# Performance work log

Hardware: AMD Instinct MI355X
Metric: run time of the kernel (lower is better)

Reference implementation:

```python
import jax, jax.numpy as jnp
import numpy as np

D_MODEL = 1024
EXPAND = 2
D_INNER = EXPAND * D_MODEL          # 2048
D_STATE = 64
NGROUPS = 1
HEADDIM = 128
NHEADS = D_INNER // HEADDIM         # 16
D_CONV = 4
CONV_DIM = D_INNER + 2 * NGROUPS * D_STATE      # 2176
D_IN_PROJ = 2 * D_INNER + 2 * NGROUPS * D_STATE + NHEADS  # 4240
BATCH = 2
SEQLEN = 4096
RMS_EPS = 1e-5


def setup_inputs() -> dict:
    key = jax.random.key(0)
    ks = jax.random.split(key, 8)
    u = jax.random.normal(ks[0], (BATCH, SEQLEN, D_MODEL), jnp.float32)
    in_proj_w = jax.random.normal(ks[1], (D_IN_PROJ, D_MODEL), jnp.float32) * 0.02
    conv_w = jax.random.normal(ks[2], (CONV_DIM, D_CONV), jnp.float32) * 0.2
    conv_b = jax.random.normal(ks[3], (CONV_DIM,), jnp.float32) * 0.1
    dt_bias = jax.random.normal(ks[4], (NHEADS,), jnp.float32) * 0.5
    # A ~ Uniform(1,16), A_log = log(A)  (as in Mamba2 init)
    A_log = jnp.log(jax.random.uniform(ks[5], (NHEADS,), jnp.float32, 1.0, 16.0))
    D = jnp.ones((NHEADS,), jnp.float32)
    rms_w = jnp.ones((D_INNER,), jnp.float32)
    out_w = jax.random.normal(ks[6], (D_MODEL, D_INNER), jnp.float32) * 0.02
    return {"u": u, "in_proj_w": in_proj_w, "conv_w": conv_w, "conv_b": conv_b,
            "dt_bias": dt_bias, "A_log": A_log, "D": D, "rms_w": rms_w, "out_w": out_w}


def reference(u, in_proj_w, conv_w, conv_b, dt_bias, A_log, D, rms_w, out_w):
    Bsz, L, _ = u.shape
    # in_proj: (B,L,d_model) -> (B,L,d_in_proj), split [z, x, B, C, dt]
    zxbcdt = jnp.einsum('bld,ed->ble', u, in_proj_w)
    s1 = D_INNER
    s2 = 2 * D_INNER
    s3 = s2 + NGROUPS * D_STATE
    s4 = s3 + NGROUPS * D_STATE
    z = zxbcdt[..., :s1]
    x = zxbcdt[..., s1:s2]
    B_part = zxbcdt[..., s2:s3]
    C_part = zxbcdt[..., s3:s4]
    dt = zxbcdt[..., s4:]
    dt = jax.nn.softplus(dt + dt_bias)            # (B,L,H), dt_limit=(0,inf) -> no clamp

    # depthwise causal conv1d + silu over [x, B, C]
    xBC = jnp.concatenate([x, B_part, C_part], axis=-1)      # (B,L,CONV_DIM)
    xt = xBC.transpose(0, 2, 1)                              # (B,C,L)
    kern = conv_w[:, None, :]                                # (C,1,W)
    conv = jax.lax.conv_general_dilated(
        xt, kern, (1,), [(D_CONV - 1, 0)],
        dimension_numbers=('NCH', 'OIH', 'NCH'),
        feature_group_count=CONV_DIM)
    xBC = jax.nn.silu((conv + conv_b[None, :, None]).transpose(0, 2, 1))

    x_c = xBC[..., :D_INNER]
    B_c = xBC[..., D_INNER:D_INNER + NGROUPS * D_STATE]
    C_c = xBC[..., D_INNER + NGROUPS * D_STATE:]
    x_s = x_c.reshape(Bsz, L, NHEADS, HEADDIM)               # (B,L,H,P)
    hpg = NHEADS // NGROUPS
    B_full = jnp.repeat(B_c.reshape(Bsz, L, NGROUPS, D_STATE), hpg, axis=2)  # (B,L,H,N)
    C_full = jnp.repeat(C_c.reshape(Bsz, L, NGROUPS, D_STATE), hpg, axis=2)

    A = -jnp.exp(A_log)                                      # (H,)

    def step(state, inp):
        x_t, dt_t, B_t, C_t = inp  # (B,H,P),(B,H),(B,H,N),(B,H,N)
        decay = jnp.exp(dt_t * A)[:, :, None, None]          # (B,H,1,1)
        state = decay * state + B_t[:, :, None, :] * x_t[..., None]  # (B,H,P,N)
        y_t = jnp.einsum('bhpn,bhn->bhp', state, C_t)
        return state, y_t

    init = jnp.zeros((Bsz, NHEADS, HEADDIM, D_STATE), u.dtype)
    xs = (x_s.transpose(1, 0, 2, 3), dt.transpose(1, 0, 2),
          B_full.transpose(1, 0, 2, 3), C_full.transpose(1, 0, 2, 3))
    _, ys = jax.lax.scan(step, init, xs)                     # (L,B,H,P)
    y = ys.transpose(1, 0, 2, 3) + D[None, None, :, None] * x_s

    y_flat = y.reshape(Bsz, L, D_INNER)
    mu = jnp.mean(y_flat * y_flat, axis=-1, keepdims=True)
    y_flat = y_flat * jax.lax.rsqrt(mu + RMS_EPS) * rms_w    # RMSNorm
    y_flat = y_flat * jax.nn.sigmoid(z)                      # gate
    return jnp.einsum('bld,ed->ble', y_flat, out_w)          # out_proj (no bias)
```

## Files before the change

kernel.cpp:

```cpp
#include <hip/hip_runtime.h>
#include <math.h>

#define D_MODEL   1024
#define D_INNER   2048
#define D_STATE   64
#define HEADDIM   128
#define NHEADS    16
#define D_CONV    4
#define BATCH     2
#define SEQLEN    4096
#define RMS_EPS   1e-5f
#define D_IN_PROJ 4240

#define ZX_LD     4224

#define LCHUNK    128
#define NCHUNK    (SEQLEN / LCHUNK)

typedef __attribute__((ext_vector_type(8))) short short8;
typedef __attribute__((ext_vector_type(4))) float f32x4;
typedef _Float16 half8 __attribute__((ext_vector_type(8)));

__device__ __forceinline__ ushort f2bf(float f) {
  unsigned u = __float_as_uint(f);
  u += 0x7fff + ((u >> 16) & 1);
  return (ushort)(u >> 16);
}
__device__ __forceinline__ float bf2f(ushort h) {
  return __uint_as_float(((unsigned)h) << 16);
}
__device__ __forceinline__ ushort f2h(float f) {
  _Float16 h = (_Float16)f;
  ushort u; __builtin_memcpy(&u, &h, 2); return u;
}
__device__ __forceinline__ void ld4(const float* p, float* d) {
  float4 v = *(const float4*)p; d[0] = v.x; d[1] = v.y; d[2] = v.z; d[3] = v.w;
}
__device__ __forceinline__ void ld4b(const ushort* p, float* d) {
  ushort4 v = *(const ushort4*)p;
  d[0] = bf2f(v.x); d[1] = bf2f(v.y); d[2] = bf2f(v.z); d[3] = bf2f(v.w);
}

__device__ __forceinline__ void gl_lds16(const ushort* g, ushort* l) {
  __builtin_amdgcn_global_load_lds(
      (const __attribute__((address_space(1))) unsigned int*)g,
      (__attribute__((address_space(3))) unsigned int*)l, 16, 0, 0);
}

__global__ void cvt_split(const float* __restrict__ w,
                          ushort* __restrict__ hi, ushort* __restrict__ lo, int n4) {
  int i = blockIdx.x * 256 + threadIdx.x;
  if (i >= n4) return;
  float4 v = ((const float4*)w)[i];
  ushort h0 = f2bf(v.x), h1 = f2bf(v.y), h2 = f2bf(v.z), h3 = f2bf(v.w);
  ushort l0 = f2bf(v.x - bf2f(h0)), l1 = f2bf(v.y - bf2f(h1));
  ushort l2 = f2bf(v.z - bf2f(h2)), l3 = f2bf(v.w - bf2f(h3));
  ((ushort4*)hi)[i] = make_ushort4(h0, h1, h2, h3);
  ((ushort4*)lo)[i] = make_ushort4(l0, l1, l2, l3);
}

__global__ void cvt_f16(const float* __restrict__ w, ushort* __restrict__ o, int n4) {
  int i = blockIdx.x * 256 + threadIdx.x;
  if (i >= n4) return;
  float4 v = ((const float4*)w)[i];
  ((ushort4*)o)[i] = make_ushort4(f2h(v.x), f2h(v.y), f2h(v.z), f2h(v.w));
}

template<int BM, int BK, bool ALO, bool OBF16>
__launch_bounds__(256, 3)
__global__ void gemm_bf16p(const ushort* __restrict__ Ah, const ushort* __restrict__ Al,
                           const ushort* __restrict__ Bh, const ushort* __restrict__ Bl,
                           float* __restrict__ C, int ldc,
                           int M, int N, int ldab, int Kslice, int n1term) {
  constexpr int BN = 128;
  constexpr int NQ = BK / 8;
  constexpr int RT = BM / 32;
  constexpr int CT = 4;
  constexpr int KS = BK / 32;

  __shared__ ushort As[ALO ? 2 : 1][BM * BK];
  __shared__ ushort Bs[2][BN * BK];

  const int bn   = blockIdx.x * BN;
  if (bn >= N) return;
  const bool two = (bn >= n1term);
  const int t    = threadIdx.x;
  const int bm   = blockIdx.y * BM;
  const int kz   = blockIdx.z;
  const int kb   = kz * Kslice;
  C += (size_t)kz * M * ldc;
  const int wave = t >> 6, lane = t & 63;
  const int ml   = lane & 15, g4 = lane >> 4;
  const int sw   = ml & (NQ - 1);
  const int wr   = wave & 1, wc = wave >> 1;
  const int r0   = wr * RT * 16, c0 = wc * CT * 16;

  f32x4 acc[RT][CT];
#pragma unroll
  for (int i = 0; i < RT; ++i)
#pragma unroll
    for (int j = 0; j < CT; ++j) acc[i][j] = (f32x4){0.f, 0.f, 0.f, 0.f};

  for (int k0 = kb; k0 < kb + Kslice; k0 += BK) {
    __syncthreads();
#pragma unroll
    for (int ii = 0; ii < BM * NQ / 256; ++ii) {
      int idx = t + ii * 256;
      int row = idx / NQ, qs = idx % NQ;
      int qg  = qs ^ (row & (NQ - 1));
      size_t go = (size_t)(bm + row) * ldab + k0 + qg * 8;
      gl_lds16(Ah + go, &As[0][idx * 8]);
      if (ALO) gl_lds16(Al + go, &As[ALO ? 1 : 0][idx * 8]);
    }
#pragma unroll
    for (int ii = 0; ii < BN * NQ / 256; ++ii) {
      int idx = t + ii * 256;
      int row = idx / NQ, qs = idx % NQ;
      int qg  = qs ^ (row & (NQ - 1));
      size_t go = (size_t)(bn + row) * ldab + k0 + qg * 8;
      gl_lds16(Bh + go, &Bs[0][idx * 8]);
      if (two) gl_lds16(Bl + go, &Bs[1][idx * 8]);
    }
    __syncthreads();

#pragma unroll
    for (int ks = 0; ks < KS; ++ks) {
      const int qA = ((ks * 4 + g4) ^ sw) * 8;
      short8 ah[RT], al[RT], bh[CT], bl[CT];
#pragma unroll
      for (int i = 0; i < RT; ++i) {
        int off = (r0 + i * 16 + ml) * BK + qA;
        ah[i] = *(const short8*)&As[0][off];
        if (ALO) al[i] = *(const short8*)&As[ALO ? 1 : 0][off];
      }
#pragma unroll
      for (int j = 0; j < CT; ++j) {
        int off = (c0 + j * 16 + ml) * BK + qA;
        bh[j] = *(const short8*)&Bs[0][off];
        if (two) bl[j] = *(const short8*)&Bs[1][off];
      }
#pragma unroll
      for (int i = 0; i < RT; ++i)
#pragma unroll
        for (int j = 0; j < CT; ++j) {
          acc[i][j] = __builtin_amdgcn_mfma_f32_16x16x32_bf16(ah[i], bh[j], acc[i][j], 0, 0, 0);
          if (two)
            acc[i][j] = __builtin_amdgcn_mfma_f32_16x16x32_bf16(ah[i], bl[j], acc[i][j], 0, 0, 0);
          if (ALO)
            acc[i][j] = __builtin_amdgcn_mfma_f32_16x16x32_bf16(al[i], bh[j], acc[i][j], 0, 0, 0);
        }
    }
  }

#pragma unroll
  for (int i = 0; i < RT; ++i)
#pragma unroll
    for (int j = 0; j < CT; ++j) {
      int col = bn + c0 + j * 16 + ml;
      if (col < N) {
        int rowb = bm + r0 + i * 16 + g4 * 4;
#pragma unroll
        for (int r = 0; r < 4; ++r) {
          if (OBF16) ((ushort*)C)[(size_t)(rowb + r) * ldc + col] = f2bf(acc[i][j][r]);
          else       C[(size_t)(rowb + r) * ldc + col] = acc[i][j][r];
        }
      }
    }
}

template<int BM, int BK, bool OBF16, bool PIPE>
__launch_bounds__(256, PIPE ? 2 : 4)
__global__ void gemm_f16(const ushort* __restrict__ Ah, const ushort* __restrict__ Bh,
                         float* __restrict__ C, int ldc,
                         int M, int N, int ldab, int Kslice) {
  constexpr int BN = 128;
  constexpr int NQ = BK / 8;
  constexpr int RT = BM / 32;
  constexpr int CT = 4;
  constexpr int KS = BK / 32;
  constexpr int NBUF = PIPE ? 2 : 1;

  __shared__ ushort As[NBUF][BM * BK];
  __shared__ ushort Bs[NBUF][BN * BK];

  const int bn   = blockIdx.x * BN;
  if (bn >= N) return;
  const int t    = threadIdx.x;
  const int bm   = blockIdx.y * BM;
  const int kz   = blockIdx.z;
  const int kb   = kz * Kslice;
  C += (size_t)kz * M * ldc;
  const int wave = t >> 6, lane = t & 63;
  const int ml   = lane & 15, g4 = lane >> 4;
  const int sw   = ml & (NQ - 1);
  const int wr   = wave & 1, wc = wave >> 1;
  const int r0   = wr * RT * 16, c0 = wc * CT * 16;

  f32x4 acc[RT][CT];
#pragma unroll
  for (int i = 0; i < RT; ++i)
#pragma unroll
    for (int j = 0; j < CT; ++j) acc[i][j] = (f32x4){0.f, 0.f, 0.f, 0.f};

  auto stage = [&](int k0, int buf) {
#pragma unroll
    for (int ii = 0; ii < BM * NQ / 256; ++ii) {
      int idx = t + ii * 256;
      int row = idx / NQ, qs = idx % NQ;
      int qg  = qs ^ (row & (NQ - 1));
      size_t go = (size_t)(bm + row) * ldab + k0 + qg * 8;
      gl_lds16(Ah + go, &As[buf][idx * 8]);
    }
#pragma unroll
    for (int ii = 0; ii < BN * NQ / 256; ++ii) {
      int idx = t + ii * 256;
      int row = idx / NQ, qs = idx % NQ;
      int qg  = qs ^ (row & (NQ - 1));
      size_t go = (size_t)(bn + row) * ldab + k0 + qg * 8;
      gl_lds16(Bh + go, &Bs[buf][idx * 8]);
    }
  };

  auto compute = [&](int buf) {
#pragma unroll
    for (int ks = 0; ks < KS; ++ks) {
      const int qA = ((ks * 4 + g4) ^ sw) * 8;
      half8 ah[RT], bh[CT];
#pragma unroll
      for (int i = 0; i < RT; ++i)
        ah[i] = *(const half8*)&As[buf][(r0 + i * 16 + ml) * BK + qA];
#pragma unroll
      for (int j = 0; j < CT; ++j)
        bh[j] = *(const half8*)&Bs[buf][(c0 + j * 16 + ml) * BK + qA];
#pragma unroll
      for (int i = 0; i < RT; ++i)
#pragma unroll
        for (int j = 0; j < CT; ++j)
          acc[i][j] = __builtin_amdgcn_mfma_f32_16x16x32_f16(ah[i], bh[j], acc[i][j], 0, 0, 0);
    }
  };

  if (PIPE) {
    const int NIT = Kslice / BK;
    stage(kb, 0);
    if (NIT > 1) stage(kb + BK, 1);
    for (int it = 0; it < NIT; ++it) {
      const int buf = it & 1;
      if (it + 1 < NIT) asm volatile("s_waitcnt vmcnt(8)" ::: "memory");
      else              asm volatile("s_waitcnt vmcnt(0)" ::: "memory");
      __builtin_amdgcn_s_barrier();
      __builtin_amdgcn_sched_barrier(0);
      compute(buf);
      __builtin_amdgcn_sched_barrier(0);
      __builtin_amdgcn_s_barrier();
      __builtin_amdgcn_sched_barrier(0);
      if (it + 2 < NIT) stage(kb + (it + 2) * BK, buf);
    }
  } else {
    for (int k0 = kb; k0 < kb + Kslice; k0 += BK) {
      __syncthreads();
      stage(k0, 0);
      __syncthreads();
      compute(0);
    }
  }

#pragma unroll
  for (int i = 0; i < RT; ++i)
#pragma unroll
    for (int j = 0; j < CT; ++j) {
      int col = bn + c0 + j * 16 + ml;
      if (col < N) {
        int rowb = bm + r0 + i * 16 + g4 * 4;
#pragma unroll
        for (int r = 0; r < 4; ++r) {
          if (OBF16) ((ushort*)C)[(size_t)(rowb + r) * ldc + col] = f2bf(acc[i][j][r]);
          else       C[(size_t)(rowb + r) * ldc + col] = acc[i][j][r];
        }
      }
    }
}

__global__ void add_out(const float* __restrict__ P, float* __restrict__ out, int n4) {
  int i = blockIdx.x * 256 + threadIdx.x;
  if (i >= n4) return;
  float4 a = ((const float4*)P)[i];
  float4 b = ((const float4*)(P + (size_t)SEQLEN * D_MODEL))[i];
  ((float4*)out)[i] = make_float4(a.x + b.x, a.y + b.y, a.z + b.z, a.w + b.w);
}

__global__ void add_dt(const float* __restrict__ P, float* __restrict__ dtb) {
  int i = blockIdx.x * 256 + threadIdx.x;
  if (i >= SEQLEN * NHEADS / 4) return;
  float4 s = ((const float4*)P)[i];
#pragma unroll
  for (int k = 1; k < 8; ++k) {
    float4 v = ((const float4*)(P + (size_t)k * SEQLEN * NHEADS))[i];
    s.x += v.x; s.y += v.y; s.z += v.z; s.w += v.w;
  }
  ((float4*)dtb)[i] = s;
}


__device__ __forceinline__ void cum_scan(float* cum, float v, int t, float* carry) {
  int lane = t & 63;
#pragma unroll
  for (int off = 1; off < 64; off <<= 1) {
    float o = __shfl_up(v, off);
    if (lane >= off) v += o;
  }
  if (t == 63) *carry = v;
  __syncthreads();
  if (t >= 64 && t < LCHUNK) v += *carry;
  if (t < LCHUNK) cum[t] = v;
  __syncthreads();
}

__device__ __forceinline__ void conv4b(const ushort* __restrict__ zx,
                                       const float* __restrict__ cw,
                                       const float* __restrict__ cb,
                                       int l, int col0, float* outv) {
  const ushort* bp = zx + (size_t)l * ZX_LD + col0;
  float r3[4], r2[4], r1[4], r0[4], bb[4];
  ld4b(bp, r3);
  if (l >= 1) ld4b(bp - ZX_LD, r2);     else { r2[0]=r2[1]=r2[2]=r2[3]=0.f; }
  if (l >= 2) ld4b(bp - 2 * ZX_LD, r1); else { r1[0]=r1[1]=r1[2]=r1[3]=0.f; }
  if (l >= 3) ld4b(bp - 3 * ZX_LD, r0); else { r0[0]=r0[1]=r0[2]=r0[3]=0.f; }
  const int ch = col0 - 2048;
  ld4(cb + ch, bb);
#pragma unroll
  for (int j = 0; j < 4; ++j) {
    float w4[4]; ld4(cw + (ch + j) * 4, w4);
    float a = bb[j];
    a = fmaf(w4[0], r0[j], a);
    a = fmaf(w4[1], r1[j], a);
    a = fmaf(w4[2], r2[j], a);
    a = fmaf(w4[3], r3[j], a);
    outv[j] = a / (1.f + __expf(-a));
  }
}

__launch_bounds__(256, 2)
__global__ void passA_ssd(const ushort* __restrict__ zx,
                          const float* __restrict__ dtb,
                          const float* __restrict__ cw, const float* __restrict__ cb,
                          const float* __restrict__ dt_bias,
                          const float* __restrict__ A_log,
                          float* __restrict__ Sc, float* __restrict__ Pc,
                          float* __restrict__ xconv, float* __restrict__ bconv) {
  const int blk = blockIdx.x;
  const int c   = blk & (NCHUNK - 1);
  const int h   = blk >> 5;
  const int l0  = c * LCHUNK;
  const int t   = threadIdx.x;
  const int wave = t >> 6, lane = t & 63;
  const int ml = lane & 15, g4 = lane >> 4;
  const float Ah = -expf(A_log[h]);

  __shared__ float cum[LCHUNK];
  __shared__ float carry;
  __shared__ ushort Xt[2][LCHUNK * 40];
  __shared__ ushort Bt[2][D_STATE * 40];

  {
    float v = 0.f;
    if (t < LCHUNK) {
      float xv = dtb[(size_t)(l0 + t) * NHEADS + h] + dt_bias[h];
      float sp = (xv > 20.f) ? xv : log1pf(expf(xv));
      v = sp * Ah;
    }
    cum_scan(cum, v, t, &carry);
  }
  const float cend = cum[LCHUNK - 1];

  f32x4 acc[2][4];
#pragma unroll
  for (int i = 0; i < 2; ++i)
#pragma unroll
    for (int j = 0; j < 4; ++j) acc[i][j] = (f32x4){0.f, 0.f, 0.f, 0.f};
  const int p0 = wave * 32;

  for (int slab = 0; slab < 4; ++slab) {
    __syncthreads();
    for (int i = 0; i < 4; ++i) {
      int q = t + i * 256;
      int s = q >> 5, p4 = (q & 31) * 4;
      int l = l0 + slab * 32 + s;
      float xv[4];
      conv4b(zx, cw, cb, l, 2048 + h * HEADDIM + p4, xv);
      *(float4*)(xconv + (size_t)l * D_INNER + h * HEADDIM + p4) =
          make_float4(xv[0], xv[1], xv[2], xv[3]);
#pragma unroll
      for (int j = 0; j < 4; ++j) {
        ushort hh = f2bf(xv[j]);
        Xt[0][(p4 + j) * 40 + s] = hh;
        Xt[1][(p4 + j) * 40 + s] = f2bf(xv[j] - bf2f(hh));
      }
    }
    for (int i = 0; i < 2; ++i) {
      int q = t + i * 256;
      int s = q >> 4, n4 = (q & 15) * 4;
      int l = l0 + slab * 32 + s;
      float wd = __expf(cend - cum[slab * 32 + s]);
      float bv[4];
      conv4b(zx, cw, cb, l, 4096 + n4, bv);
      if (h == 0)
        *(float4*)(bconv + (size_t)l * D_STATE + n4) =
            make_float4(bv[0], bv[1], bv[2], bv[3]);
#pragma unroll
      for (int j = 0; j < 4; ++j) {
        float val = bv[j] * wd;
        ushort hh = f2bf(val);
        Bt[0][(n4 + j) * 40 + s] = hh;
        Bt[1][(n4 + j) * 40 + s] = f2bf(val - bf2f(hh));
      }
    }
    __syncthreads();

    short8 xa_h[2], xa_l[2];
#pragma unroll
    for (int pi = 0; pi < 2; ++pi) {
      int off = (p0 + pi * 16 + ml) * 40 + g4 * 8;
      xa_h[pi] = *(const short8*)&Xt[0][off];
      xa_l[pi] = *(const short8*)&Xt[1][off];
    }
#pragma unroll
    for (int ni = 0; ni < 4; ++ni) {
      int off = (ni * 16 + ml) * 40 + g4 * 8;
      short8 bh = *(const short8*)&Bt[0][off];
      short8 bl = *(const short8*)&Bt[1][off];
#pragma unroll
      for (int pi = 0; pi < 2; ++pi) {
        acc[pi][ni] = __builtin_amdgcn_mfma_f32_16x16x32_bf16(xa_h[pi], bh, acc[pi][ni], 0, 0, 0);
        acc[pi][ni] = __builtin_amdgcn_mfma_f32_16x16x32_bf16(xa_h[pi], bl, acc[pi][ni], 0, 0, 0);
        acc[pi][ni] = __builtin_amdgcn_mfma_f32_16x16x32_bf16(xa_l[pi], bh, acc[pi][ni], 0, 0, 0);
      }
    }
  }

  float* S = Sc + (size_t)blk * (HEADDIM * D_STATE);
#pragma unroll
  for (int pi = 0; pi < 2; ++pi)
#pragma unroll
    for (int ni = 0; ni < 4; ++ni) {
      int n = ni * 16 + ml;
#pragma unroll
      for (int r = 0; r < 4; ++r) {
        int p = p0 + pi * 16 + g4 * 4 + r;
        S[(size_t)p * D_STATE + n] = acc[pi][ni][r];
      }
    }
  if (t == 0) Pc[blk] = __expf(cend);
}

__global__ void scan_passB(float* __restrict__ Sc, const float* __restrict__ Pc) {
  const int h = blockIdx.x;
  const int e = blockIdx.y * 512 + threadIdx.x;
  const size_t hb = (size_t)h * NCHUNK;
  float st = 0.f;
  for (int c = 0; c < NCHUNK; ++c) {
    size_t idx = (hb + c) * (HEADDIM * D_STATE) + e;
    float P = Pc[hb + c];
    float v = Sc[idx];
    Sc[idx] = st;
    st = fmaf(P, st, v);
  }
}

__launch_bounds__(256, 2)
__global__ void passC_ssd(const ushort* __restrict__ zx,
                          const float* __restrict__ dtb,
                          const float* __restrict__ cw, const float* __restrict__ cb,
                          const float* __restrict__ dt_bias,
                          const float* __restrict__ A_log,
                          const float* __restrict__ Dp,
                          const float* __restrict__ Sc,
                          const float* __restrict__ bconv,
                          float* __restrict__ ybuf) {
  const int blk = blockIdx.x;
  const int c   = blk & (NCHUNK - 1);
  const int h   = blk >> 5;
  const int l0  = c * LCHUNK;
  const int t   = threadIdx.x;
  const int wave = t >> 6, lane = t & 63;
  const int ml = lane & 15, g4 = lane >> 4;
  const int t0 = wave * 32;
  const float Ah = -expf(A_log[h]);
  const float Dh = Dp[h];

  __shared__ float cum[LCHUNK];
  __shared__ float carry;
  __shared__ ushort Bsl[2][2][32 * 40];
  __shared__ ushort Msl[2][LCHUNK * 40];
  __shared__ ushort Xt[2][LCHUNK * 40];

  {
    float v = 0.f;
    if (t < LCHUNK) {
      float xv = dtb[(size_t)(l0 + t) * NHEADS + h] + dt_bias[h];
      float sp = (xv > 20.f) ? xv : log1pf(expf(xv));
      v = sp * Ah;
    }
    cum_scan(cum, v, t, &carry);
  }

  short8 c_h[2][2], c_l[2][2];
  {
    ushort* CSh = &Msl[0][0];
    ushort* CSl = &Xt[0][0];
    int row = t >> 1, half = t & 1;
    int l = l0 + row;
    int colbase = 4160 + half * 32;
#pragma unroll
    for (int j0 = 0; j0 < 32; j0 += 4) {
      float cv[4];
      conv4b(zx, cw, cb, l, colbase + j0, cv);
      int colc = half * 32 + j0;
      int quad = colc >> 3;
      int addr = row * 64 + ((quad ^ (row & 7)) << 3) + (colc & 7);
      ushort h0 = f2bf(cv[0]), h1 = f2bf(cv[1]), h2 = f2bf(cv[2]), h3 = f2bf(cv[3]);
      *(ushort4*)&CSh[addr] = make_ushort4(h0, h1, h2, h3);
      *(ushort4*)&CSl[addr] = make_ushort4(
          f2bf(cv[0] - bf2f(h0)), f2bf(cv[1] - bf2f(h1)),
          f2bf(cv[2] - bf2f(h2)), f2bf(cv[3] - bf2f(h3)));
    }
    __syncthreads();
#pragma unroll
    for (int ks = 0; ks < 2; ++ks)
#pragma unroll
      for (int ti = 0; ti < 2; ++ti) {
        int rw = t0 + ti * 16 + ml;
        int ad = rw * 64 + (((ks * 4 + g4) ^ (rw & 7)) << 3);
        c_h[ks][ti] = *(const short8*)&CSh[ad];
        c_l[ks][ti] = *(const short8*)&CSl[ad];
      }
  }

  f32x4 accY[2][8];
#pragma unroll
  for (int i = 0; i < 2; ++i)
#pragma unroll
    for (int j = 0; j < 8; ++j) accY[i][j] = (f32x4){0.f, 0.f, 0.f, 0.f};

  const float* xcv = ybuf;

  for (int slab = 0; slab < 4; ++slab) {
    __syncthreads();
#pragma unroll
    for (int i = 0; i < 2; ++i) {
      int q = t + i * 256;
      int s = q >> 4, n4 = (q & 15) * 4;
      int l = l0 + slab * 32 + s;
      float4 v = *(const float4*)(bconv + (size_t)l * D_STATE + n4);
      float bv[4] = {v.x, v.y, v.z, v.w};
      int ks = n4 >> 5, jj = n4 & 31;
      ushort h0 = f2bf(bv[0]), h1 = f2bf(bv[1]), h2 = f2bf(bv[2]), h3 = f2bf(bv[3]);
      *(ushort4*)&Bsl[ks][0][s * 40 + jj] = make_ushort4(h0, h1, h2, h3);
      *(ushort4*)&Bsl[ks][1][s * 40 + jj] = make_ushort4(
          f2bf(bv[0] - bf2f(h0)), f2bf(bv[1] - bf2f(h1)),
          f2bf(bv[2] - bf2f(h2)), f2bf(bv[3] - bf2f(h3)));
    }
#pragma unroll
    for (int i = 0; i < 4; ++i) {
      int q = t + i * 256;
      int p = q & 127, sg = q >> 7;
      ushort hh[4], ll[4];
#pragma unroll
      for (int j = 0; j < 4; ++j) {
        int l = l0 + slab * 32 + sg * 4 + j;
        float xv = xcv[(size_t)l * D_INNER + h * HEADDIM + p];
        hh[j] = f2bf(xv);
        ll[j] = f2bf(xv - bf2f(hh[j]));
      }
      *(ushort4*)&Xt[0][p * 40 + sg * 4] = make_ushort4(hh[0], hh[1], hh[2], hh[3]);
      *(ushort4*)&Xt[1][p * 40 + sg * 4] = make_ushort4(ll[0], ll[1], ll[2], ll[3]);
    }
    __syncthreads();

    if (wave >= slab) {
      f32x4 g[2][2];
#pragma unroll
      for (int i = 0; i < 2; ++i)
#pragma unroll
        for (int j = 0; j < 2; ++j) g[i][j] = (f32x4){0.f, 0.f, 0.f, 0.f};
#pragma unroll
      for (int ks = 0; ks < 2; ++ks) {
#pragma unroll
        for (int si = 0; si < 2; ++si) {
          int off = (si * 16 + ml) * 40 + g4 * 8;
          short8 bh = *(const short8*)&Bsl[ks][0][off];
          short8 bl = *(const short8*)&Bsl[ks][1][off];
#pragma unroll
          for (int ti = 0; ti < 2; ++ti) {
            g[ti][si] = __builtin_amdgcn_mfma_f32_16x16x32_bf16(c_h[ks][ti], bh, g[ti][si], 0, 0, 0);
            g[ti][si] = __builtin_amdgcn_mfma_f32_16x16x32_bf16(c_h[ks][ti], bl, g[ti][si], 0, 0, 0);
            g[ti][si] = __builtin_amdgcn_mfma_f32_16x16x32_bf16(c_l[ks][ti], bh, g[ti][si], 0, 0, 0);
          }
        }
      }
#pragma unroll
      for (int ti = 0; ti < 2; ++ti)
#pragma unroll
        for (int si = 0; si < 2; ++si) {
          int sl = si * 16 + ml;
          int sg = slab * 32 + sl;
#pragma unroll
          for (int r = 0; r < 4; ++r) {
            int tg = t0 + ti * 16 + g4 * 4 + r;
            float coeff = (sg <= tg) ? __expf(cum[tg] - cum[sg]) : 0.f;
            float val = g[ti][si][r] * coeff + ((sg == tg) ? Dh : 0.f);
            ushort hh = f2bf(val);
            Msl[0][tg * 40 + sl] = hh;
            Msl[1][tg * 40 + sl] = f2bf(val - bf2f(hh));
          }
        }
      asm volatile("s_waitcnt lgkmcnt(0)" ::: "memory");
      short8 ma_h[2], ma_l[2];
#pragma unroll
      for (int ti = 0; ti < 2; ++ti) {
        int off = (t0 + ti * 16 + ml) * 40 + g4 * 8;
        ma_h[ti] = *(const short8*)&Msl[0][off];
        ma_l[ti] = *(const short8*)&Msl[1][off];
      }
#pragma unroll
      for (int pi = 0; pi < 8; ++pi) {
        int off = (pi * 16 + ml) * 40 + g4 * 8;
        short8 xh = *(const short8*)&Xt[0][off];
        short8 xl = *(const short8*)&Xt[1][off];
#pragma unroll
        for (int ti = 0; ti < 2; ++ti) {
          accY[ti][pi] = __builtin_amdgcn_mfma_f32_16x16x32_bf16(ma_h[ti], xh, accY[ti][pi], 0, 0, 0);
          accY[ti][pi] = __builtin_amdgcn_mfma_f32_16x16x32_bf16(ma_h[ti], xl, accY[ti][pi], 0, 0, 0);
          accY[ti][pi] = __builtin_amdgcn_mfma_f32_16x16x32_bf16(ma_l[ti], xh, accY[ti][pi], 0, 0, 0);
        }
      }
    }
  }

  const float* S = Sc + (size_t)blk * (HEADDIM * D_STATE);
#pragma unroll
  for (int ns = 0; ns < 2; ++ns) {
    __syncthreads();
#pragma unroll
    for (int i = 0; i < 4; ++i) {
      int q = t + i * 256;
      int p = q >> 3, j4 = (q & 7) * 4;
      float4 v = *(const float4*)(S + (size_t)p * D_STATE + ns * 32 + j4);
      float vv[4] = {v.x, v.y, v.z, v.w};
      ushort hh0 = f2bf(vv[0]), hh1 = f2bf(vv[1]), hh2 = f2bf(vv[2]), hh3 = f2bf(vv[3]);
      *(ushort4*)&Xt[0][p * 40 + j4] = make_ushort4(hh0, hh1, hh2, hh3);
      *(ushort4*)&Xt[1][p * 40 + j4] =
          make_ushort4(f2bf(vv[0] - bf2f(hh0)), f2bf(vv[1] - bf2f(hh1)),
                       f2bf(vv[2] - bf2f(hh2)), f2bf(vv[3] - bf2f(hh3)));
    }
    __syncthreads();
    short8 ma_h[2], ma_l[2];
#pragma unroll
    for (int ti = 0; ti < 2; ++ti) {
      float e = __expf(cum[t0 + ti * 16 + ml]);
#pragma unroll
      for (int j = 0; j < 8; ++j) {
        float v = (bf2f((ushort)c_h[ns][ti][j]) + bf2f((ushort)c_l[ns][ti][j])) * e;
        ushort hh = f2bf(v);
        ma_h[ti][j] = (short)hh;
        ma_l[ti][j] = (short)f2bf(v - bf2f(hh));
      }
    }
#pragma unroll
    for (int pi = 0; pi < 8; ++pi) {
      int off = (pi * 16 + ml) * 40 + g4 * 8;
      short8 xh = *(const short8*)&Xt[0][off];
      short8 xl = *(const short8*)&Xt[1][off];
#pragma unroll
      for (int ti = 0; ti < 2; ++ti) {
        accY[ti][pi] = __builtin_amdgcn_mfma_f32_16x16x32_bf16(ma_h[ti], xh, accY[ti][pi], 0, 0, 0);
        accY[ti][pi] = __builtin_amdgcn_mfma_f32_16x16x32_bf16(ma_h[ti], xl, accY[ti][pi], 0, 0, 0);
        accY[ti][pi] = __builtin_amdgcn_mfma_f32_16x16x32_bf16(ma_l[ti], xh, accY[ti][pi], 0, 0, 0);
      }
    }
  }

#pragma unroll
  for (int ti = 0; ti < 2; ++ti)
#pragma unroll
    for (int pi = 0; pi < 8; ++pi) {
      int p = pi * 16 + ml;
#pragma unroll
      for (int r = 0; r < 4; ++r) {
        int l = l0 + t0 + ti * 16 + g4 * 4 + r;
        ybuf[(size_t)l * D_INNER + h * HEADDIM + p] = accY[ti][pi][r];
      }
    }
}

__launch_bounds__(256)
__global__ void rmsnorm_gate_split(const float* __restrict__ ybuf,
                                   const ushort* __restrict__ zx,
                                   const float* __restrict__ rms_w,
                                   ushort* __restrict__ yh) {
  const int row = blockIdx.x;
  const int t   = threadIdx.x;
  const float* y  = ybuf + (size_t)row * D_INNER;
  const ushort* z = zx   + (size_t)row * ZX_LD;

  float4 a  = *(const float4*)(y + t * 8);
  float4 bq = *(const float4*)(y + t * 8 + 4);
  float ss = a.x * a.x + a.y * a.y + a.z * a.z + a.w * a.w +
             bq.x * bq.x + bq.y * bq.y + bq.z * bq.z + bq.w * bq.w;
#pragma unroll
  for (int off = 32; off > 0; off >>= 1) ss += __shfl_down(ss, off);
  __shared__ float red[4];
  if ((t & 63) == 0) red[t >> 6] = ss;
  __syncthreads();
  float tot = red[0] + red[1] + red[2] + red[3];
  float scale = rsqrtf(tot * (1.f / (float)D_INNER) + RMS_EPS);

  float vy[8] = {a.x, a.y, a.z, a.w, bq.x, bq.y, bq.z, bq.w};
  ushort4 zv0 = *(const ushort4*)(z + t * 8);
  ushort4 zv1 = *(const ushort4*)(z + t * 8 + 4);
  ushort zz[8] = {zv0.x, zv0.y, zv0.z, zv0.w, zv1.x, zv1.y, zv1.z, zv1.w};
  ushort hh[8];
#pragma unroll
  for (int jj = 0; jj < 8; ++jj) {
    int col = t * 8 + jj;
    float g = 1.f / (1.f + __expf(-bf2f(zz[jj])));
    float v = vy[jj] * scale * rms_w[col] * g;
    hh[jj] = f2h(v);
  }
  size_t o = (size_t)row * D_INNER + t * 8;
  *(ushort4*)(yh + o)     = make_ushort4(hh[0], hh[1], hh[2], hh[3]);
  *(ushort4*)(yh + o + 4) = make_ushort4(hh[4], hh[5], hh[6], hh[7]);
}

extern "C" void kernel_launch(void* const* d_in, const int* in_sizes, int n_in,
                              void* d_out, int out_size, void* d_ws, size_t ws_size,
                              hipStream_t stream) {
  const float* u         = (const float*)d_in[0];
  const float* in_proj_w = (const float*)d_in[1];
  const float* conv_w    = (const float*)d_in[2];
  const float* conv_b    = (const float*)d_in[3];
  const float* dt_bias   = (const float*)d_in[4];
  const float* A_log     = (const float*)d_in[5];
  const float* Dp        = (const float*)d_in[6];
  const float* rms_w     = (const float*)d_in[7];
  const float* out_w     = (const float*)d_in[8];
  float* out = (float*)d_out;

  float* ws    = (float*)d_ws;
  ushort* zxbc = (ushort*)ws;
  float* dtb   = ws   + (size_t)SEQLEN * ZX_LD / 2;
  float* dtp   = dtb  + (size_t)SEQLEN * NHEADS;
  float* ybuf  = dtp  + (size_t)8 * SEQLEN * NHEADS;
  float* Pc    = ybuf + (size_t)SEQLEN * D_INNER;
  float* Sc    = Pc   + 512;
  ushort* uh   = (ushort*)(Sc + (size_t)NHEADS * NCHUNK * HEADDIM * D_STATE);
  ushort* ul   = uh  + (size_t)SEQLEN * D_MODEL;
  ushort* w1h  = ul  + (size_t)SEQLEN * D_MODEL;
  ushort* w1l  = w1h + (size_t)D_IN_PROJ * D_MODEL;
  ushort* w2h  = w1l + (size_t)D_IN_PROJ * D_MODEL;
  ushort* w2l  = w2h + (size_t)D_MODEL * D_INNER;
  ushort* yh   = (ushort*)Sc;
  float* Opart = ybuf;
  float* bconv = dtp;
  ushort* uf16 = (ushort*)ybuf;

  {
    int n4 = D_IN_PROJ * D_MODEL / 4;
    cvt_split<<<(n4 + 255) / 256, 256, 0, stream>>>(in_proj_w, w1h, w1l, n4);
    int z4 = ZX_LD * D_MODEL / 4;
    cvt_f16<<<(z4 + 255) / 256, 256, 0, stream>>>(in_proj_w, w1h, z4);
    int m4 = D_MODEL * D_INNER / 4;
    cvt_f16<<<(m4 + 255) / 256, 256, 0, stream>>>(out_w, w2h, m4);
  }

  for (int b = 0; b < BATCH; ++b) {
    const float* u_b  = u   + (size_t)b * SEQLEN * D_MODEL;
    float*      out_b = out + (size_t)b * SEQLEN * D_MODEL;

    {
      int n4 = SEQLEN * D_MODEL / 4;
      cvt_split<<<(n4 + 255) / 256, 256, 0, stream>>>(u_b, uh, ul, n4);
      cvt_f16<<<(n4 + 255) / 256, 256, 0, stream>>>(u_b, uf16, n4);
    }

    {
      dim3 g(40, SEQLEN / 128, 1);
      gemm_f16<128, 64, true, false><<<g, 256, 0, stream>>>(uf16, w1h, (float*)zxbc,
                                                            ZX_LD, SEQLEN, ZX_LD,
                                                            D_MODEL, D_MODEL);
    }
    {
      const ushort* bh = w1h + (size_t)ZX_LD * D_MODEL;
      const ushort* bl = w1l + (size_t)ZX_LD * D_MODEL;
      dim3 g(1, SEQLEN / 128, 8);
      gemm_bf16p<128, 32, true, false><<<g, 256, 0, stream>>>(uh, ul, bh, bl,
                                                          dtp, NHEADS, SEQLEN, NHEADS,
                                                          D_MODEL, D_MODEL / 8, 0);
      add_dt<<<(SEQLEN * NHEADS / 4 + 255) / 256, 256, 0, stream>>>(dtp, dtb);
    }

    passA_ssd<<<NHEADS * NCHUNK, 256, 0, stream>>>(zxbc, dtb, conv_w, conv_b,
                                                   dt_bias, A_log, Sc, Pc,
                                                   ybuf, bconv);
    scan_passB<<<dim3(NHEADS, (HEADDIM * D_STATE) / 512), 512, 0, stream>>>(Sc, Pc);
    passC_ssd<<<NHEADS * NCHUNK, 256, 0, stream>>>(zxbc, dtb, conv_w, conv_b,
                                                   dt_bias, A_log, Dp, Sc,
                                                   bconv, ybuf);

    rmsnorm_gate_split<<<SEQLEN, 256, 0, stream>>>(ybuf, zxbc, rms_w, yh);

    {
      dim3 g(D_MODEL / 128, SEQLEN / 128, 2);
      gemm_f16<128, 64, false, true><<<g, 256, 0, stream>>>(yh, w2h, Opart, D_MODEL,
                                                            SEQLEN, D_MODEL,
                                                            D_INNER, D_INNER / 2);
    }
    add_out<<<(SEQLEN * D_MODEL / 4 + 255) / 256, 256, 0, stream>>>(Opart, out_b,
                                                                    SEQLEN * D_MODEL / 4);
  }
}
```

Before: 522.6 us.

## Use 256x256-tile double-buffered GEMM for bulk of in_proj, remainder with old kernel

Replaces the 128x128-tile in_proj GEMM (z/x/B/C columns) with a new 512-thread 256x256 tile kernel that double-buffers LDS loads and raises per-block data reuse. It covers the first 4096 output columns, and the remaining 128 columns are handled by the existing kernel through a new column-offset parameter. The larger tile lowers global/LDS traffic per FLOP but uses 128KB of LDS and many accumulator registers, which limits occupancy, and the grid shrinks to 256 blocks.

```diff
diff --git a/kernel.cpp b/kernel.cpp
--- a/kernel.cpp
+++ b/kernel.cpp
@@ -172,7 +172,7 @@
 __launch_bounds__(256, PIPE ? 2 : 4)
 __global__ void gemm_f16(const ushort* __restrict__ Ah, const ushort* __restrict__ Bh,
                          float* __restrict__ C, int ldc,
-                         int M, int N, int ldab, int Kslice) {
+                         int M, int N, int ldab, int Kslice, int bn0) {
   constexpr int BN = 128;
   constexpr int NQ = BK / 8;
   constexpr int RT = BM / 32;
@@ -183,7 +183,7 @@
   __shared__ ushort As[NBUF][BM * BK];
   __shared__ ushort Bs[NBUF][BN * BK];
 
-  const int bn   = blockIdx.x * BN;
+  const int bn   = bn0 + blockIdx.x * BN;
   if (bn >= N) return;
   const int t    = threadIdx.x;
   const int bm   = blockIdx.y * BM;
@@ -278,6 +278,87 @@
           else       C[(size_t)(rowb + r) * ldc + col] = acc[i][j][r];
         }
       }
+    }
+}
+
+__launch_bounds__(512, 2)
+__global__ void gemm_f16_256(const ushort* __restrict__ Ah, const ushort* __restrict__ Bh,
+                             ushort* __restrict__ C, int ldc, int ldab, int K) {
+  __shared__ ushort As[2][256 * 64];
+  __shared__ ushort Bs[2][256 * 64];
+
+  const int t    = threadIdx.x;
+  const int bn   = blockIdx.x * 256;
+  const int bm   = blockIdx.y * 256;
+  const int wave = t >> 6, lane = t & 63;
+  const int wr   = wave >> 2, wc = wave & 3;
+  const int ml   = lane & 15, g4 = lane >> 4;
+  const int sw   = ml & 7;
+
+  f32x4 acc[8][4];
+#pragma unroll
+  for (int i = 0; i < 8; ++i)
+#pragma unroll
+    for (int j = 0; j < 4; ++j) acc[i][j] = (f32x4){0.f, 0.f, 0.f, 0.f};
+
+  auto stage = [&](int k0, int buf) {
+#pragma unroll
+    for (int ii = 0; ii < 4; ++ii) {
+      int idx = t + ii * 512;
+      int row = idx >> 3, qs = idx & 7;
+      int qg  = qs ^ (row & 7);
+      gl_lds16(Ah + (size_t)(bm + row) * ldab + k0 + qg * 8, &As[buf][idx * 8]);
+    }
+#pragma unroll
+    for (int ii = 0; ii < 4; ++ii) {
+      int idx = t + ii * 512;
+      int row = idx >> 3, qs = idx & 7;
+      int qg  = qs ^ (row & 7);
+      gl_lds16(Bh + (size_t)(bn + row) * ldab + k0 + qg * 8, &Bs[buf][idx * 8]);
+    }
+  };
+
+  const int NIT = K / 64;
+  stage(0, 0);
+
+  for (int it = 0; it < NIT; ++it) {
+    const int buf = it & 1;
+    __syncthreads();
+    if (it + 1 < NIT) stage((it + 1) * 64, buf ^ 1);
+
+    half8 bfr[4][2];
+#pragma unroll
+    for (int ni = 0; ni < 4; ++ni)
+#pragma unroll
+      for (int ks = 0; ks < 2; ++ks) {
+        int qA = ((ks * 4 + g4) ^ sw) * 8;
+        bfr[ni][ks] = *(const half8*)&Bs[buf][(wc * 64 + ni * 16 + ml) * 64 + qA];
+      }
+#pragma unroll
+    for (int mi = 0; mi < 8; ++mi) {
+      half8 af[2];
+#pragma unroll
+      for (int ks = 0; ks < 2; ++ks) {
+        int qA = ((ks * 4 + g4) ^ sw) * 8;
+        af[ks] = *(const half8*)&As[buf][(wr * 128 + mi * 16 + ml) * 64 + qA];
+      }
+#pragma unroll
+      for (int ks = 0; ks < 2; ++ks)
+#pragma unroll
+        for (int ni = 0; ni < 4; ++ni)
+          acc[mi][ni] = __builtin_amdgcn_mfma_f32_16x16x32_f16(af[ks], bfr[ni][ks], acc[mi][ni], 0, 0, 0);
+    }
+  }
+
+#pragma unroll
+  for (int mi = 0; mi < 8; ++mi)
+#pragma unroll
+    for (int ni = 0; ni < 4; ++ni) {
+      int col = bn + wc * 64 + ni * 16 + ml;
+      int rowb = bm + wr * 128 + mi * 16 + g4 * 4;
+#pragma unroll
+      for (int r = 0; r < 4; ++r)
+        C[(size_t)(rowb + r) * ldc + col] = f2bf(acc[mi][ni][r]);
     }
 }
 
@@ -784,10 +865,12 @@
     }
 
     {
-      dim3 g(40, SEQLEN / 128, 1);
-      gemm_f16<128, 64, true, false><<<g, 256, 0, stream>>>(uf16, w1h, (float*)zxbc,
-                                                            ZX_LD, SEQLEN, ZX_LD,
-                                                            D_MODEL, D_MODEL);
+      dim3 g(16, 16, 1);
+      gemm_f16_256<<<g, 512, 0, stream>>>(uf16, w1h, zxbc, ZX_LD, D_MODEL, D_MODEL);
+      dim3 gr(1, SEQLEN / 128, 1);
+      gemm_f16<128, 64, true, false><<<gr, 256, 0, stream>>>(uf16, w1h, (float*)zxbc,
+                                                             ZX_LD, SEQLEN, ZX_LD,
+                                                             D_MODEL, D_MODEL, 4096);
     }
     {
       const ushort* bh = w1h + (size_t)ZX_LD * D_MODEL;
@@ -813,7 +896,7 @@
       dim3 g(D_MODEL / 128, SEQLEN / 128, 2);
       gemm_f16<128, 64, false, true><<<g, 256, 0, stream>>>(yh, w2h, Opart, D_MODEL,
                                                             SEQLEN, D_MODEL,
-                                                            D_INNER, D_INNER / 2);
+                                                            D_INNER, D_INNER / 2, 0);
     }
     add_out<<<(SEQLEN * D_MODEL / 4 + 255) / 256, 256, 0, stream>>>(Opart, out_b,
                                                                     SEQLEN * D_MODEL / 4);
```

Measured after the change: 533.7 us. +2.1%, slower.
